# Performance work log

Hardware: AMD Instinct MI355X
Metric: run time of the kernel (lower is better)

## Reference

```python
import jax, jax.numpy as jnp
import numpy as np

B, S, D, H = 4, 1024, 512, 8
DH = D // H  # 64 head dim; max_len == S for the masked (preceding_only) skew path


def setup_inputs() -> dict:
    key = jax.random.key(0)
    ks = jax.random.split(key, 8)
    queries = jax.random.normal(ks[0], (B, S, D), jnp.float32)
    keys_ = jax.random.normal(ks[1], (B, S, D), jnp.float32)
    values = jax.random.normal(ks[2], (B, S, D), jnp.float32)
    Wq = jax.random.normal(ks[3], (D, D), jnp.float32) * 0.03
    Wk = jax.random.normal(ks[4], (D, D), jnp.float32) * 0.03
    Wv = jax.random.normal(ks[5], (D, D), jnp.float32) * 0.03
    Wo = jax.random.normal(ks[6], (D, D), jnp.float32) * 0.03
    rel_emb = jax.random.normal(ks[7], (H, DH, S), jnp.float32) * 0.03  # preceding_only -> len == max_len
    i = jnp.arange(S)
    mask = jnp.where(i[None, :] > i[:, None], -1e9, 0.0).astype(jnp.float32)[None, None]  # [1,1,S,S] causal
    return {"queries": queries, "keys": keys_, "values": values, "mask": mask,
            "Wq": Wq, "Wk": Wk, "Wv": Wv, "Wo": Wo, "rel_emb": rel_emb}


def _skewed_rel_bias(q, rel_emb):
    # q: [B,H,S,DH], rel_emb: [H,DH,L] with L == max_len == S
    b, h, s, _ = q.shape
    L = rel_emb.shape[-1]
    qe = jnp.einsum('bhsd,hdl->bhsl', q, rel_emb)  # [B,H,S,L]
    # _qe_masking: keep qe[..., i, j] where j >= L-1-i
    lengths = (L - 1) - jnp.arange(s)
    keep = (jnp.arange(L)[None, :] >= lengths[:, None]).astype(qe.dtype)
    qe = qe * keep
    # skew: pad one column on the left, fold into [B,H,L+1,S], drop first row
    qe = jnp.pad(qe, ((0, 0), (0, 0), (0, 0), (1, 0)))
    qe = qe.reshape(b, h, L + 1, s)[:, :, 1:, :]  # [B,H,L,S]
    return qe


def reference(queries, keys, values, mask, Wq, Wk, Wv, Wo, rel_emb):
    b, s, _ = queries.shape
    h, dh, _ = rel_emb.shape
    scale = dh ** -0.5

    def split(x):  # [B,S,H*DH] -> [B,H,S,DH]
        return x.reshape(b, s, h, dh).transpose(0, 2, 1, 3)

    q = split(queries @ Wq)
    k = split(keys @ Wk)
    v = split(values @ Wv)

    logits = jnp.einsum('bhsd,bhtd->bhst', q, k)
    logits = logits + _skewed_rel_bias(q, rel_emb)
    logits = (logits + mask[:, :, :s, :s]) * scale  # original scales after adding mask
    weights = jax.nn.softmax(logits, axis=-1)
    ctx = jnp.einsum('bhst,bhtd->bhsd', weights, v)
    ctx = ctx.transpose(0, 2, 1, 3).reshape(b, s, h * dh)
    return ctx @ Wo
```

## Files before the change

kernel.cpp:

```cpp
#include <hip/hip_runtime.h>
#include <hip/hip_bf16.h>

#define SB 4
#define SS 1024
#define SD 512
#define SH 8
#define SDH 64

typedef short bf16x8 __attribute__((ext_vector_type(8)));
typedef float f32x4 __attribute__((ext_vector_type(4)));

#define MFMA(a, b, c) __builtin_amdgcn_mfma_f32_16x16x32_bf16(a, b, c, 0, 0, 0)

__device__ __forceinline__ void load_lds16(const void* g, void* l) {
  __builtin_amdgcn_global_load_lds(
      (__attribute__((address_space(1))) void*)(const_cast<void*>(g)),
      (__attribute__((address_space(3))) void*)(l), 16, 0, 0);
}

__global__ __launch_bounds__(256) void k_prep(
    const float* __restrict__ q, const float* __restrict__ k, const float* __restrict__ v,
    const float* __restrict__ Wq, const float* __restrict__ Wk, const float* __restrict__ Wv,
    const float* __restrict__ Wo, const float* __restrict__ rel,
    __hip_bfloat16* __restrict__ Xq, __hip_bfloat16* __restrict__ Xk,
    __hip_bfloat16* __restrict__ Xv, __hip_bfloat16* __restrict__ Wqt,
    __hip_bfloat16* __restrict__ Wkt, __hip_bfloat16* __restrict__ Wvt,
    __hip_bfloat16* __restrict__ Wot, __hip_bfloat16* __restrict__ relT) {
  __shared__ float tile[32][33];
  const int y = blockIdx.y, x = blockIdx.x, t = threadIdx.x;
  if (y < 3) {
    const float2* in = (const float2*)(y == 0 ? q : y == 1 ? k : v);
    __hip_bfloat162* out = (__hip_bfloat162*)(y == 0 ? Xq : y == 1 ? Xk : Xv);
    const int n2 = SB * SS * SD / 2;
    int i = x * 256 + t, st = 512 * 256;
    for (; i < n2; i += st) out[i] = __float22bfloat162_rn(in[i]);
    return;
  }
  int tx = t & 31, ty = t >> 5;
  if (y < 5) {
    int which = (y - 3) * 2 + (x >> 8), idx = x & 255;
    const float* ip = which == 0 ? Wq : which == 1 ? Wk : which == 2 ? Wv : Wo;
    __hip_bfloat16* op = which == 0 ? Wqt : which == 1 ? Wkt : which == 2 ? Wvt : Wot;
    int c0 = (idx & 15) * 32, r0 = (idx >> 4) * 32;
    for (int rr = ty; rr < 32; rr += 8) tile[rr][tx] = ip[(size_t)(r0 + rr) * SD + c0 + tx];
    __syncthreads();
    for (int cc = ty; cc < 32; cc += 8)
      op[(size_t)(c0 + cc) * SD + r0 + tx] = __float2bfloat16(tile[tx][cc]);
    return;
  }
  int hd = x >> 6, idx = x & 63;
  int c0 = (idx >> 1) * 32, r0 = (idx & 1) * 32;
  const float* ip = rel + (size_t)hd * SDH * SS;
  __hip_bfloat16* op = relT + (size_t)hd * SDH * SS;
  for (int rr = ty; rr < 32; rr += 8) tile[rr][tx] = ip[(size_t)(r0 + rr) * SS + c0 + tx];
  __syncthreads();
  for (int cc = ty; cc < 32; cc += 8)
    op[(size_t)(c0 + cc) * SDH + r0 + tx] = __float2bfloat16(tile[tx][cc]);
}

__device__ __forceinline__ void gemm_core(const __hip_bfloat16* __restrict__ A,
                                          const __hip_bfloat16* __restrict__ Bt,
                                          void* __restrict__ Cout, int mode) {
  __shared__ __hip_bfloat16 As[128 * 64];
  __shared__ __hip_bfloat16 Bs[64 * 64];
  const int t = threadIdx.x, w = t >> 6, lane = t & 63;
  const int quad = lane >> 4, l16 = lane & 15;
  const int m0 = blockIdx.y * 128, n0 = blockIdx.x * 64;
  const int wm = (w >> 1) * 64, wn = (w & 1) * 32;
  f32x4 zero4 = {0.0f, 0.0f, 0.0f, 0.0f};
  f32x4 acc[4][2];
#pragma unroll
  for (int mi = 0; mi < 4; ++mi)
#pragma unroll
    for (int nj = 0; nj < 2; ++nj) acc[mi][nj] = zero4;

  for (int kt = 0; kt < SD; kt += 64) {
#pragma unroll
    for (int c = 0; c < 4; ++c) {
      int ofs = c * 256 + t;
      int row = ofs >> 3, col = (ofs & 7) ^ (row & 7);
      load_lds16(A + (size_t)(m0 + row) * SD + kt + col * 8,
                 (char*)As + (size_t)(c * 256 + w * 64) * 16);
    }
#pragma unroll
    for (int c = 0; c < 2; ++c) {
      int ofs = c * 256 + t;
      int row = ofs >> 3, col = (ofs & 7) ^ (row & 7);
      load_lds16(Bt + (size_t)(n0 + row) * SD + kt + col * 8,
                 (char*)Bs + (size_t)(c * 256 + w * 64) * 16);
    }
    __syncthreads();
    bf16x8 af[4][2], bfr[2][2];
#pragma unroll
    for (int mi = 0; mi < 4; ++mi) {
      int row = wm + mi * 16 + l16;
#pragma unroll
      for (int ks = 0; ks < 2; ++ks)
        af[mi][ks] = *(const bf16x8*)((const char*)As + row * 128 +
                                      ((ks * 4 + quad) ^ (row & 7)) * 16);
    }
#pragma unroll
    for (int nj = 0; nj < 2; ++nj) {
      int row = wn + nj * 16 + l16;
#pragma unroll
      for (int ks = 0; ks < 2; ++ks)
        bfr[nj][ks] = *(const bf16x8*)((const char*)Bs + row * 128 +
                                       ((ks * 4 + quad) ^ (row & 7)) * 16);
    }
#pragma unroll
    for (int mi = 0; mi < 4; ++mi)
#pragma unroll
      for (int nj = 0; nj < 2; ++nj) {
        acc[mi][nj] = MFMA(af[mi][0], bfr[nj][0], acc[mi][nj]);
        acc[mi][nj] = MFMA(af[mi][1], bfr[nj][1], acc[mi][nj]);
      }
    __syncthreads();
  }
#pragma unroll
  for (int mi = 0; mi < 4; ++mi)
#pragma unroll
    for (int nj = 0; nj < 2; ++nj)
#pragma unroll
      for (int r = 0; r < 4; ++r) {
        int m = m0 + wm + mi * 16 + quad * 4 + r;
        int n = n0 + wn + nj * 16 + l16;
        float v = acc[mi][nj][r];
        if (mode == 2) {
          ((float*)Cout)[(size_t)m * SD + n] = v;
        } else {
          int b = m >> 10, s = m & 1023, hh = n >> 6, dh = n & 63;
          __hip_bfloat16 bv = __float2bfloat16(v);
          if (mode == 0)
            ((__hip_bfloat16*)Cout)[((size_t)(b * SH + hh) * SS + s) * SDH + dh] = bv;
          else
            ((__hip_bfloat16*)Cout)[((size_t)(b * SH + hh) * SDH + dh) * SS + s] = bv;
        }
      }
}

__global__ __launch_bounds__(256) void k_gemm_qkv(
    const __hip_bfloat16* __restrict__ Xq, const __hip_bfloat16* __restrict__ Xk,
    const __hip_bfloat16* __restrict__ Xv, const __hip_bfloat16* __restrict__ Wqt,
    const __hip_bfloat16* __restrict__ Wkt, const __hip_bfloat16* __restrict__ Wvt,
    __hip_bfloat16* __restrict__ Qb, __hip_bfloat16* __restrict__ Kb,
    __hip_bfloat16* __restrict__ Vt) {
  int z = blockIdx.z;
  const __hip_bfloat16* A = z == 0 ? Xq : z == 1 ? Xk : Xv;
  const __hip_bfloat16* Bt = z == 0 ? Wqt : z == 1 ? Wkt : Wvt;
  void* C = z == 0 ? (void*)Qb : z == 1 ? (void*)Kb : (void*)Vt;
  gemm_core(A, Bt, C, z == 2 ? 1 : 0);
}

__global__ __launch_bounds__(256) void k_gemm_o(const __hip_bfloat16* __restrict__ CTX,
                                                const __hip_bfloat16* __restrict__ Wot,
                                                float* __restrict__ Out) {
  gemm_core(CTX, Wot, Out, 2);
}

__device__ const int TTm[40] = {0,1,2,3,4,4,5,5,6,6,7,7,8,8,8,9,9,9,10,10,10,11,11,11,
                                12,12,12,12,13,13,13,13,14,14,14,14,15,15,15,15};
__device__ const int CCm[40] = {0,0,0,0,0,1,0,1,0,1,0,1,0,1,2,0,1,2,0,1,2,0,1,2,
                                0,1,2,3,0,1,2,3,0,1,2,3,0,1,2,3};

__global__ __launch_bounds__(256) void k_flash(const __hip_bfloat16* __restrict__ Qb,
                                               const __hip_bfloat16* __restrict__ Kb,
                                               const __hip_bfloat16* __restrict__ Vt,
                                               const __hip_bfloat16* __restrict__ relT,
                                               float* __restrict__ Opart,
                                               float* __restrict__ lpart) {
  __shared__ __hip_bfloat16 Klds[64 * 64];
  __shared__ __hip_bfloat16 Vlds[64 * 64];
  __shared__ __hip_bfloat16 REs[128 * 64];
  __shared__ __hip_bfloat16 QEP[64 * 136];
  const int t = threadIdx.x, w = t >> 6, lane = t & 63;
  const int quad = lane >> 4, l16 = lane & 15;
  const int idx = blockIdx.x, bh = blockIdx.y, h = bh & 7;
  const int tI = TTm[idx], c = CCm[idx];
  const int i0 = tI * 64;
  const int rem = tI + 1 - c * 4;
  const int nt = rem < 4 ? rem : 4;
  const size_t qbase = (size_t)bh * SS * SDH;
  const __hip_bfloat16* Rp = relT + (size_t)h * SS * SDH;

  const int qrow = i0 + w * 16 + l16;
  bf16x8 qf0 = *(const bf16x8*)(Qb + qbase + (size_t)qrow * SDH + quad * 8);
  bf16x8 qf1 = *(const bf16x8*)(Qb + qbase + (size_t)qrow * SDH + 32 + quad * 8);

  f32x4 zero4 = {0.0f, 0.0f, 0.0f, 0.0f};
  f32x4 acc_o[4];
#pragma unroll
  for (int dt = 0; dt < 4; ++dt) acc_o[dt] = zero4;
  float ls[4] = {0.0f, 0.0f, 0.0f, 0.0f};
  const int rloc = quad * 4;
  __hip_bfloat16* myrow = QEP + (size_t)(w * 16 + rloc) * 136;

  for (int jt = 0; jt < nt; ++jt) {
    const int jtile = c * 4 + jt, j0 = jtile * 64;
    const int l0 = 960 - 64 * (tI - jtile);
#pragma unroll
    for (int cc = 0; cc < 2; ++cc) {
      int ofs = cc * 256 + t;
      int row = ofs >> 3, col = (ofs & 7) ^ (row & 7);
      load_lds16(Kb + qbase + (size_t)(j0 + row) * SDH + col * 8,
                 (char*)Klds + (size_t)(cc * 256 + w * 64) * 16);
      load_lds16(Vt + (size_t)bh * SDH * SS + (size_t)row * SS + j0 + col * 8,
                 (char*)Vlds + (size_t)(cc * 256 + w * 64) * 16);
    }
#pragma unroll
    for (int cc = 0; cc < 4; ++cc) {
      int ofs = cc * 256 + t;
      int row = ofs >> 3, col = (ofs & 7) ^ (row & 7);
      int lr = l0 + row;
      if (lr > 1023) lr = 1023;
      load_lds16(Rp + (size_t)lr * SDH + col * 8,
                 (char*)REs + (size_t)(cc * 256 + w * 64) * 16);
    }
    __syncthreads();

    f32x4 s[4];
#pragma unroll
    for (int nj = 0; nj < 4; ++nj) {
      int row = nj * 16 + l16;
      bf16x8 b0 = *(const bf16x8*)((const char*)Klds + row * 128 + (quad ^ (row & 7)) * 16);
      bf16x8 b1 = *(const bf16x8*)((const char*)Klds + row * 128 + ((4 + quad) ^ (row & 7)) * 16);
      f32x4 z = zero4;
      z = MFMA(qf0, b0, z);
      z = MFMA(qf1, b1, z);
      s[nj] = z;
    }
#pragma unroll
    for (int nc = 0; nc < 8; ++nc) {
      int row = nc * 16 + l16;
      bf16x8 b0 = *(const bf16x8*)((const char*)REs + row * 128 + (quad ^ (row & 7)) * 16);
      bf16x8 b1 = *(const bf16x8*)((const char*)REs + row * 128 + ((4 + quad) ^ (row & 7)) * 16);
      f32x4 e = zero4;
      e = MFMA(qf0, b0, e);
      e = MFMA(qf1, b1, e);
#pragma unroll
      for (int r = 0; r < 4; ++r)
        myrow[r * 136 + nc * 16 + l16] = __float2bfloat16(e[r]);
    }

#pragma unroll
    for (int nj = 0; nj < 4; ++nj) {
      int jc = nj * 16 + l16, jcol = j0 + jc;
#pragma unroll
      for (int r = 0; r < 4; ++r) {
        int irow = i0 + w * 16 + rloc + r;
        float bias = __bfloat162float(myrow[r * 136 + 63 + jc - (rloc + r)]);
        float val = (s[nj][r] + bias) * 0.125f - 8.0f;
        float p = (jcol <= irow) ? __expf(val) : 0.0f;
        s[nj][r] = p;
        ls[r] += p;
      }
    }
#pragma unroll
    for (int nj = 0; nj < 4; ++nj)
#pragma unroll
      for (int r = 0; r < 4; ++r)
        myrow[r * 136 + nj * 16 + l16] = __float2bfloat16(s[nj][r]);

#pragma unroll
    for (int js = 0; js < 2; ++js) {
      bf16x8 pa = *(const bf16x8*)(QEP + (size_t)(w * 16 + l16) * 136 + js * 32 + quad * 8);
#pragma unroll
      for (int dt = 0; dt < 4; ++dt) {
        int row = dt * 16 + l16;
        bf16x8 vb = *(const bf16x8*)((const char*)Vlds + row * 128 +
                                     ((js * 4 + quad) ^ (row & 7)) * 16);
        acc_o[dt] = MFMA(pa, vb, acc_o[dt]);
      }
    }
    __syncthreads();
  }
  const size_t pbase = (size_t)(bh * 16 + tI) * 4 + c;
  float* Op = Opart + pbase * 4096;
#pragma unroll
  for (int r = 0; r < 4; ++r) {
    float sum = ls[r];
    sum += __shfl_xor(sum, 1, 64);
    sum += __shfl_xor(sum, 2, 64);
    sum += __shfl_xor(sum, 4, 64);
    sum += __shfl_xor(sum, 8, 64);
    int row = w * 16 + rloc + r;
#pragma unroll
    for (int dt = 0; dt < 4; ++dt) Op[row * 64 + dt * 16 + l16] = acc_o[dt][r];
    if (l16 == 0) lpart[pbase * 64 + row] = sum;
  }
}

__global__ __launch_bounds__(256) void k_reduce(const float* __restrict__ Opart,
                                                const float* __restrict__ lpart,
                                                __hip_bfloat16* __restrict__ CTX) {
  const int tI = blockIdx.x, bh = blockIdx.y, b = bh >> 3, h = bh & 7;
  const int nc = tI / 4 + 1;
  const int tid = threadIdx.x;
  __shared__ float lsum[64];
  const size_t base = (size_t)(bh * 16 + tI) * 4;
  if (tid < 64) {
    float s = 0.0f;
    for (int cc = 0; cc < nc; ++cc) s += lpart[(base + cc) * 64 + tid];
    lsum[tid] = s;
  }
  __syncthreads();
  const int e0 = tid * 16;
  const int row = e0 >> 6, d0 = e0 & 63;
  float4 o[4] = {};
  for (int cc = 0; cc < nc; ++cc) {
    const float4* p = (const float4*)(Opart + (base + cc) * 4096);
#pragma unroll
    for (int vv = 0; vv < 4; ++vv) {
      float4 x = p[tid * 4 + vv];
      o[vv].x += x.x; o[vv].y += x.y; o[vv].z += x.z; o[vv].w += x.w;
    }
  }
  const float rl = 1.0f / lsum[row];
  __hip_bfloat16* op = CTX + ((size_t)b * SS + tI * 64 + row) * SD + h * SDH + d0;
#pragma unroll
  for (int vv = 0; vv < 4; ++vv) {
    op[vv * 4 + 0] = __float2bfloat16(o[vv].x * rl);
    op[vv * 4 + 1] = __float2bfloat16(o[vv].y * rl);
    op[vv * 4 + 2] = __float2bfloat16(o[vv].z * rl);
    op[vv * 4 + 3] = __float2bfloat16(o[vv].w * rl);
  }
}

extern "C" void kernel_launch(void* const* d_in, const int* in_sizes, int n_in,
                              void* d_out, int out_size, void* d_ws, size_t ws_size,
                              hipStream_t stream) {
  const float* queries = (const float*)d_in[0];
  const float* keys    = (const float*)d_in[1];
  const float* values  = (const float*)d_in[2];
  const float* Wq = (const float*)d_in[4];
  const float* Wk = (const float*)d_in[5];
  const float* Wv = (const float*)d_in[6];
  const float* Wo = (const float*)d_in[7];
  const float* rel = (const float*)d_in[8];

  char* ws = (char*)d_ws;
  size_t off = 0;
  auto alloc = [&](size_t bytes) {
    char* p = ws + off;
    off += (bytes + 255) & ~(size_t)255;
    return p;
  };
  const size_t XB = (size_t)SB * SS * SD * 2;
  const size_t WB = (size_t)SD * SD * 2;
  __hip_bfloat16* Wqt  = (__hip_bfloat16*)alloc(WB);
  __hip_bfloat16* Wkt  = (__hip_bfloat16*)alloc(WB);
  __hip_bfloat16* Wvt  = (__hip_bfloat16*)alloc(WB);
  __hip_bfloat16* Wot  = (__hip_bfloat16*)alloc(WB);
  __hip_bfloat16* relT = (__hip_bfloat16*)alloc((size_t)SH * SS * SDH * 2);
  __hip_bfloat16* Qb   = (__hip_bfloat16*)alloc(XB);
  __hip_bfloat16* Kb   = (__hip_bfloat16*)alloc(XB);
  __hip_bfloat16* Vt   = (__hip_bfloat16*)alloc(XB);
  __hip_bfloat16* CTX  = (__hip_bfloat16*)alloc(XB);
  char* uni = alloc((size_t)2048 * 4096 * 4 + (size_t)2048 * 64 * 4);
  __hip_bfloat16* Xq = (__hip_bfloat16*)uni;
  __hip_bfloat16* Xk = (__hip_bfloat16*)(uni + XB);
  __hip_bfloat16* Xv = (__hip_bfloat16*)(uni + 2 * XB);
  float* Opart = (float*)uni;
  float* lpart = (float*)(uni + (size_t)2048 * 4096 * 4);
  if (off > ws_size) return;

  k_prep<<<dim3(512, 6), dim3(256), 0, stream>>>(
      queries, keys, values, Wq, Wk, Wv, Wo, rel,
      Xq, Xk, Xv, Wqt, Wkt, Wvt, Wot, relT);
  k_gemm_qkv<<<dim3(SD / 64, SB * SS / 128, 3), dim3(256), 0, stream>>>(
      Xq, Xk, Xv, Wqt, Wkt, Wvt, Qb, Kb, Vt);
  k_flash<<<dim3(40, SB * SH), dim3(256), 0, stream>>>(Qb, Kb, Vt, relT, Opart, lpart);
  k_reduce<<<dim3(16, SB * SH), dim3(256), 0, stream>>>(Opart, lpart, CTX);
  k_gemm_o<<<dim3(SD / 64, SB * SS / 128), dim3(256), 0, stream>>>(CTX, Wot, (float*)d_out);
}
```

Measured before the change: 160.5 us.

## Coarsen causal flash split to 8-tile chunks and write unsplit rows directly

Reworks the causal work partition. The first eight query tiles are handled by one block each, and those blocks normalize and write bf16 context directly. The remaining tiles are split into two chunks of up to eight key tiles, replacing the previous four-tile chunks. This cuts the grid from 40 to 24 blocks per head and shrinks the partial-output traffic and the reduce kernel, at the cost of fewer and longer blocks that may balance less evenly across CUs.

```diff
diff --git a/kernel.cpp b/kernel.cpp
--- a/kernel.cpp
+++ b/kernel.cpp
@@ -157,17 +157,13 @@
   gemm_core(CTX, Wot, Out, 2);
 }
 
-__device__ const int TTm[40] = {0,1,2,3,4,4,5,5,6,6,7,7,8,8,8,9,9,9,10,10,10,11,11,11,
-                                12,12,12,12,13,13,13,13,14,14,14,14,15,15,15,15};
-__device__ const int CCm[40] = {0,0,0,0,0,1,0,1,0,1,0,1,0,1,2,0,1,2,0,1,2,0,1,2,
-                                0,1,2,3,0,1,2,3,0,1,2,3,0,1,2,3};
-
 __global__ __launch_bounds__(256) void k_flash(const __hip_bfloat16* __restrict__ Qb,
                                                const __hip_bfloat16* __restrict__ Kb,
                                                const __hip_bfloat16* __restrict__ Vt,
                                                const __hip_bfloat16* __restrict__ relT,
                                                float* __restrict__ Opart,
-                                               float* __restrict__ lpart) {
+                                               float* __restrict__ lpart,
+                                               __hip_bfloat16* __restrict__ CTX) {
   __shared__ __hip_bfloat16 Klds[64 * 64];
   __shared__ __hip_bfloat16 Vlds[64 * 64];
   __shared__ __hip_bfloat16 REs[128 * 64];
@@ -175,10 +171,15 @@
   const int t = threadIdx.x, w = t >> 6, lane = t & 63;
   const int quad = lane >> 4, l16 = lane & 15;
   const int idx = blockIdx.x, bh = blockIdx.y, h = bh & 7;
-  const int tI = TTm[idx], c = CCm[idx];
+  int tI, c, jt0, nt;
+  bool single;
+  if (idx < 8) {
+    tI = idx; c = 0; jt0 = 0; nt = tI + 1; single = true;
+  } else {
+    tI = 8 + ((idx - 8) >> 1); c = (idx - 8) & 1;
+    jt0 = c ? 8 : 0; nt = c ? (tI - 7) : 8; single = false;
+  }
   const int i0 = tI * 64;
-  const int rem = tI + 1 - c * 4;
-  const int nt = rem < 4 ? rem : 4;
   const size_t qbase = (size_t)bh * SS * SDH;
   const __hip_bfloat16* Rp = relT + (size_t)h * SS * SDH;
 
@@ -195,7 +196,7 @@
   __hip_bfloat16* myrow = QEP + (size_t)(w * 16 + rloc) * 136;
 
   for (int jt = 0; jt < nt; ++jt) {
-    const int jtile = c * 4 + jt, j0 = jtile * 64;
+    const int jtile = jt0 + jt, j0 = jtile * 64;
     const int l0 = 960 - 64 * (tI - jtile);
 #pragma unroll
     for (int cc = 0; cc < 2; ++cc) {
@@ -273,8 +274,7 @@
     }
     __syncthreads();
   }
-  const size_t pbase = (size_t)(bh * 16 + tI) * 4 + c;
-  float* Op = Opart + pbase * 4096;
+  float rsum[4];
 #pragma unroll
   for (int r = 0; r < 4; ++r) {
     float sum = ls[r];
@@ -282,46 +282,53 @@
     sum += __shfl_xor(sum, 2, 64);
     sum += __shfl_xor(sum, 4, 64);
     sum += __shfl_xor(sum, 8, 64);
-    int row = w * 16 + rloc + r;
-#pragma unroll
-    for (int dt = 0; dt < 4; ++dt) Op[row * 64 + dt * 16 + l16] = acc_o[dt][r];
-    if (l16 == 0) lpart[pbase * 64 + row] = sum;
-  }
-}
-
-__global__ __launch_bounds__(256) void k_reduce(const float* __restrict__ Opart,
-                                                const float* __restrict__ lpart,
-                                                __hip_bfloat16* __restrict__ CTX) {
-  const int tI = blockIdx.x, bh = blockIdx.y, b = bh >> 3, h = bh & 7;
-  const int nc = tI / 4 + 1;
-  const int tid = threadIdx.x;
+    rsum[r] = sum;
+  }
+  if (single) {
+    const int b = bh >> 3;
+#pragma unroll
+    for (int r = 0; r < 4; ++r) {
+      int row = w * 16 + rloc + r;
+      float rl = 1.0f / rsum[r];
+#pragma unroll
+      for (int dt = 0; dt < 4; ++dt)
+        CTX[((size_t)b * SS + i0 + row) * SD + h * SDH + dt * 16 + l16] =
+            __float2bfloat16(acc_o[dt][r] * rl);
+    }
+  } else {
+    const size_t pbase = ((size_t)bh * 8 + (tI - 8)) * 2 + c;
+    float* Op = Opart + pbase * 4096;
+#pragma unroll
+    for (int r = 0; r < 4; ++r) {
+      int row = w * 16 + rloc + r;
+#pragma unroll
+      for (int dt = 0; dt < 4; ++dt) Op[row * 64 + dt * 16 + l16] = acc_o[dt][r];
+      if (l16 == 0) lpart[pbase * 64 + row] = rsum[r];
+    }
+  }
+}
+
+__global__ __launch_bounds__(256) void k_reduce2(const float* __restrict__ Opart,
+                                                 const float* __restrict__ lpart,
+                                                 __hip_bfloat16* __restrict__ CTX) {
+  const int bx = blockIdx.x, bh = blockIdx.y, b = bh >> 3, h = bh & 7;
+  const int tI = 8 + bx, tid = threadIdx.x;
   __shared__ float lsum[64];
-  const size_t base = (size_t)(bh * 16 + tI) * 4;
-  if (tid < 64) {
-    float s = 0.0f;
-    for (int cc = 0; cc < nc; ++cc) s += lpart[(base + cc) * 64 + tid];
-    lsum[tid] = s;
-  }
+  const size_t base = ((size_t)bh * 8 + bx) * 2;
+  if (tid < 64) lsum[tid] = lpart[base * 64 + tid] + lpart[(base + 1) * 64 + tid];
   __syncthreads();
-  const int e0 = tid * 16;
-  const int row = e0 >> 6, d0 = e0 & 63;
-  float4 o[4] = {};
-  for (int cc = 0; cc < nc; ++cc) {
-    const float4* p = (const float4*)(Opart + (base + cc) * 4096);
-#pragma unroll
-    for (int vv = 0; vv < 4; ++vv) {
-      float4 x = p[tid * 4 + vv];
-      o[vv].x += x.x; o[vv].y += x.y; o[vv].z += x.z; o[vv].w += x.w;
-    }
-  }
+  const int e0 = tid * 16, row = e0 >> 6, d0 = e0 & 63;
+  const float4* p0 = (const float4*)(Opart + base * 4096);
+  const float4* p1 = (const float4*)(Opart + (base + 1) * 4096);
   const float rl = 1.0f / lsum[row];
   __hip_bfloat16* op = CTX + ((size_t)b * SS + tI * 64 + row) * SD + h * SDH + d0;
 #pragma unroll
   for (int vv = 0; vv < 4; ++vv) {
-    op[vv * 4 + 0] = __float2bfloat16(o[vv].x * rl);
-    op[vv * 4 + 1] = __float2bfloat16(o[vv].y * rl);
-    op[vv * 4 + 2] = __float2bfloat16(o[vv].z * rl);
-    op[vv * 4 + 3] = __float2bfloat16(o[vv].w * rl);
+    float4 x = p0[tid * 4 + vv], y = p1[tid * 4 + vv];
+    op[vv * 4 + 0] = __float2bfloat16((x.x + y.x) * rl);
+    op[vv * 4 + 1] = __float2bfloat16((x.y + y.y) * rl);
+    op[vv * 4 + 2] = __float2bfloat16((x.z + y.z) * rl);
+    op[vv * 4 + 3] = __float2bfloat16((x.w + y.w) * rl);
   }
 }
 
@@ -355,12 +362,12 @@
   __hip_bfloat16* Kb   = (__hip_bfloat16*)alloc(XB);
   __hip_bfloat16* Vt   = (__hip_bfloat16*)alloc(XB);
   __hip_bfloat16* CTX  = (__hip_bfloat16*)alloc(XB);
-  char* uni = alloc((size_t)2048 * 4096 * 4 + (size_t)2048 * 64 * 4);
+  char* uni = alloc(3 * XB);
   __hip_bfloat16* Xq = (__hip_bfloat16*)uni;
   __hip_bfloat16* Xk = (__hip_bfloat16*)(uni + XB);
   __hip_bfloat16* Xv = (__hip_bfloat16*)(uni + 2 * XB);
   float* Opart = (float*)uni;
-  float* lpart = (float*)(uni + (size_t)2048 * 4096 * 4);
+  float* lpart = (float*)(uni + (size_t)32 * 8 * 2 * 4096 * 4);
   if (off > ws_size) return;
 
   k_prep<<<dim3(512, 6), dim3(256), 0, stream>>>(
@@ -368,7 +375,7 @@
       Xq, Xk, Xv, Wqt, Wkt, Wvt, Wot, relT);
   k_gemm_qkv<<<dim3(SD / 64, SB * SS / 128, 3), dim3(256), 0, stream>>>(
       Xq, Xk, Xv, Wqt, Wkt, Wvt, Qb, Kb, Vt);
-  k_flash<<<dim3(40, SB * SH), dim3(256), 0, stream>>>(Qb, Kb, Vt, relT, Opart, lpart);
-  k_reduce<<<dim3(16, SB * SH), dim3(256), 0, stream>>>(Opart, lpart, CTX);
+  k_flash<<<dim3(24, SB * SH), dim3(256), 0, stream>>>(Qb, Kb, Vt, relT, Opart, lpart, CTX);
+  k_reduce2<<<dim3(8, SB * SH), dim3(256), 0, stream>>>(Opart, lpart, CTX);
   k_gemm_o<<<dim3(SD / 64, SB * SS / 128), dim3(256), 0, stream>>>(CTX, Wot, (float*)d_out);
 }
```

Measured after the change: 158.0 us. No clear change (-1.6%).
